# Optimization experiments

Measured on AMD Instinct MI355X. Metric: run time of the kernel, lower is better.

## Reference

```python
import jax, jax.numpy as jnp
import numpy as np

B, T, V, D = 16, 200, 25, 128
N_Q, N_E = 4, 1024
BETA, ALPHA, SLOPE, LN_EPS = 0.25, 0.1, 0.2, 1e-5

def _ring_adjacency(v):
    A = np.zeros((v, v), dtype=np.float32)
    for i in range(v):
        A[i, (i + 1) % v] = 1.0
        A[i, (i - 1) % v] = 1.0
    A = A + np.eye(v, dtype=np.float32)  # A + I, as in module
    d_inv_sqrt = 1.0 / np.sqrt(A.sum(1))
    return (d_inv_sqrt[:, None] * A) * d_inv_sqrt[None, :]

def setup_inputs() -> dict:
    key = jax.random.key(0)
    k_z, k_e, k_w = jax.random.split(key, 3)
    z = jax.random.normal(k_z, (B, T, V, D), dtype=jnp.float32)
    # xavier_uniform for each [n_e, e_dim] codebook
    lim = float(np.sqrt(6.0 / (N_E + D)))
    emb = jax.random.uniform(k_e, (N_Q, N_E, D), dtype=jnp.float32, minval=-lim, maxval=lim)
    wlim = float(np.sqrt(1.0 / D))
    gcn_w = jax.random.uniform(k_w, (D, D), dtype=jnp.float32, minval=-wlim, maxval=wlim)
    return {
        "z": z,
        "emb": emb,
        "A_norm": jnp.asarray(_ring_adjacency(V)),
        "gcn_w": gcn_w,
        "gcn_b": jnp.zeros((D,), jnp.float32),
        "ln_scale": jnp.ones((D,), jnp.float32),
        "ln_bias": jnp.zeros((D,), jnp.float32),
    }

def _gcn_refine(residual, A_norm, gcn_w, gcn_b, ln_scale, ln_bias):
    # residual: [N, V, d]
    neigh = jnp.einsum('vw,nwd->nvd', A_norm, residual)
    neigh = neigh @ gcn_w.T + gcn_b                      # nn.Linear
    neigh = jnp.where(neigh >= 0, neigh, SLOPE * neigh)  # LeakyReLU(0.2)
    mu = neigh.mean(-1, keepdims=True)
    var = ((neigh - mu) ** 2).mean(-1, keepdims=True)
    neigh = (neigh - mu) / jnp.sqrt(var + LN_EPS) * ln_scale + ln_bias
    return residual + ALPHA * neigh

def reference(z, emb, A_norm, gcn_w, gcn_b, ln_scale, ln_bias):
    b, t, v, d = z.shape
    n_q = emb.shape[0]
    zf = z.reshape(b * t, v, d)
    residual = zf
    cum = jnp.zeros_like(zf)
    losses, idxs = [], []
    for k in range(n_q):
        refined = _gcn_refine(residual, A_norm, gcn_w, gcn_b, ln_scale, ln_bias)
        W = emb[k]                               # [n_e, d]
        flat = refined.reshape(-1, d)            # [N*V, d]
        dist = ((flat ** 2).sum(1, keepdims=True)
                - 2.0 * flat @ W.T
                + (W ** 2).sum(1)[None, :])
        idx = jnp.argmin(dist, axis=1)           # [N*V]
        q = W[idx].reshape(b * t, v, d)          # == one_hot @ W
        # commit and codebook terms are identical squared errors -> (1+beta)*mse
        diff = q - jax.lax.stop_gradient(residual)
        losses.append((1.0 + BETA) * (diff ** 2).mean(-1))
        cum = cum + q
        residual = residual - q
        idxs.append(idx.reshape(b * t, v))
    zq = zf + jax.lax.stop_gradient(cum - zf)    # straight-through
    total_loss = jnp.stack(losses, 0).mean()
    indices = jnp.stack(idxs, -1).reshape(b, t, v, n_q)
    return zq.reshape(b, t, v, d), total_loss, indices
```

## Files before the change

kernel.cpp:

```cpp
#include <hip/hip_runtime.h>

#define ZQ_N    10240000
#define IDX_OFF 10240001
#define FLT_BIG 3.402823466e38f

typedef _Float16 f16x8 __attribute__((ext_vector_type(8)));
typedef float    f32x4 __attribute__((ext_vector_type(4)));

__global__ __launch_bounds__(256) void k_wsq(const float* __restrict__ emb,
                                             float* __restrict__ wsq,
                                             float* __restrict__ loss_part) {
    int t = threadIdx.x;
    int g = blockIdx.x * 256 + t;
    if (g < 1024) loss_part[g] = 0.f;
    int row = blockIdx.x * 64 + (t >> 2);
    int seg = t & 3;
    const float4* p = (const float4*)(emb + row * 128 + seg * 32);
    float a = 0.f;
#pragma unroll
    for (int i = 0; i < 8; i++) {
        float4 w = p[i];
        a = fmaf(w.x, w.x, a); a = fmaf(w.y, w.y, a);
        a = fmaf(w.z, w.z, a); a = fmaf(w.w, w.w, a);
    }
    a += __shfl_xor(a, 1);
    a += __shfl_xor(a, 2);
    if (seg == 0) wsq[row] = a;
}

__global__ __launch_bounds__(256) void k_wsplit(const float* __restrict__ emb,
        _Float16* __restrict__ wh, _Float16* __restrict__ wl,
        const float* __restrict__ gw,
        _Float16* __restrict__ gh, _Float16* __restrict__ gl) {
    int c = blockIdx.x * 256 + threadIdx.x;
    int q   = c >> 14;
    int col = (c >> 4) & 1023;
    int k8  = (c & 15) * 8;
    const float* srcp = emb + q * 131072 + col * 128 + k8;
    float4 a = *(const float4*)(srcp);
    float4 b = *(const float4*)(srcp + 4);
    float vv[8] = {a.x, a.y, a.z, a.w, b.x, b.y, b.z, b.w};
    union { _Float16 h[8]; uint4 u4; } ph, pl;
#pragma unroll
    for (int j = 0; j < 8; j++) {
        float v = vv[j] * 1024.f;
        _Float16 h = (_Float16)v;
        float r1 = v - (float)h;
        ph.h[j] = h; pl.h[j] = (_Float16)r1;
    }
    int P  = col >> 7, w = (col >> 5) & 3, ct = (col >> 4) & 1, lm = col & 15;
    int ks = k8 >> 5, quad = (k8 >> 3) & 3;
    int off = (((P * 4 + w) * 4 + ks) * 2 + ct) * 512 + (quad * 16 + lm) * 8;
    *(uint4*)(wh + q * 131072 + off) = ph.u4;
    *(uint4*)(wl + q * 131072 + off) = pl.u4;

    if (c < 16384) {
        float v = gw[c] * 1024.f;
        _Float16 h = (_Float16)v;
        float r1 = v - (float)h;
        gh[c] = h; gl[c] = (_Float16)r1;
    }
}

__global__ __launch_bounds__(256) void k_refine(const float* __restrict__ zbase,
        const float* __restrict__ emb, const float* __restrict__ idx_f, int stage,
        float* __restrict__ refined, float* __restrict__ s_out,
        const float* __restrict__ An,
        const _Float16* __restrict__ gh, const _Float16* __restrict__ gl,
        const float* __restrict__ gb, const float* __restrict__ lsc,
        const float* __restrict__ lbi) {
    __shared__ __align__(16) float Rn[25 * 128];
    __shared__ __align__(16) unsigned char nbuf[2 * 32 * 136 * 2];
    __shared__ float Al[625];
    __shared__ int cds[75];
    _Float16* nh = (_Float16*)nbuf;
    _Float16* nl = (_Float16*)(nbuf + 8704);
    float*    nei = (float*)nbuf;
    const int tid = threadIdx.x;
    const int n = blockIdx.x;

    if (tid < 75) {
        int r = tid / 3, j = tid - r * 3;
        if (j < stage) cds[tid] = (int)idx_f[(n * 25 + r) * 4 + j];
    }
    for (int i = tid; i < 625; i += 256) Al[i] = An[i];
    __syncthreads();

    const float4* zp = (const float4*)(zbase + n * 3200);
    float4* Rn4 = (float4*)Rn;
    for (int i = tid; i < 800; i += 256) {
        float4 rv = zp[i];
        int r = i >> 5, c4 = (i & 31) * 4;
#pragma unroll
        for (int j = 0; j < 3; j++) {
            if (j < stage) {
                const float4 q = *(const float4*)(emb + j * 131072 + cds[r * 3 + j] * 128 + c4);
                rv.x -= q.x; rv.y -= q.y; rv.z -= q.z; rv.w -= q.w;
            }
        }
        Rn4[i] = rv;
    }
    __syncthreads();

    for (int i = tid; i < 512; i += 256) {
        int r = i >> 4, k8 = (i & 15) * 8;
        union { _Float16 h[8]; uint4 u4; } ph, pl;
        if (r < 25) {
            int vm = (r == 0) ? 24 : r - 1;
            int vp = (r == 24) ? 0 : r + 1;
            float am = Al[r * 25 + vm], a0 = Al[r * 25 + r], ap = Al[r * 25 + vp];
#pragma unroll
            for (int j = 0; j < 8; j++) {
                int d = k8 + j;
                float val = am * Rn[vm * 128 + d];
                val = fmaf(a0, Rn[r  * 128 + d], val);
                val = fmaf(ap, Rn[vp * 128 + d], val);
                float v1 = val * 1024.f;
                _Float16 h = (_Float16)v1; float fh = (float)h;
                ph.h[j] = h; pl.h[j] = (_Float16)(v1 - fh);
            }
        } else {
            ph.u4 = make_uint4(0u, 0u, 0u, 0u);
            pl.u4 = make_uint4(0u, 0u, 0u, 0u);
        }
        int off = r * 136 + k8;
        *(uint4*)(&nh[off]) = ph.u4;
        *(uint4*)(&nl[off]) = pl.u4;
    }
    __syncthreads();

    {
        const int lane = tid & 63;
        const int wv   = tid >> 6;
        const int quad = lane >> 4;
        const int lm   = lane & 15;
        const int bbase = (wv * 32 + lm) * 128 + quad * 8;
        const int abase = lm * 136 + quad * 8;

        f32x4 racc[2][2];
#pragma unroll
        for (int a = 0; a < 2; a++)
#pragma unroll
            for (int b = 0; b < 2; b++) racc[a][b] = (f32x4){0.f, 0.f, 0.f, 0.f};

#pragma unroll
        for (int k0 = 0; k0 < 4; k0++) {
            const int ko = k0 * 32;
            f16x8 ah[2], al[2];
#pragma unroll
            for (int mt = 0; mt < 2; mt++) {
                ah[mt] = *(const f16x8*)(&nh[abase + mt * (16 * 136) + ko]);
                al[mt] = *(const f16x8*)(&nl[abase + mt * (16 * 136) + ko]);
            }
            f16x8 bh[2], bl[2];
#pragma unroll
            for (int ct = 0; ct < 2; ct++) {
                bh[ct] = *(const f16x8*)(gh + bbase + ct * (16 * 128) + ko);
                bl[ct] = *(const f16x8*)(gl + bbase + ct * (16 * 128) + ko);
            }
#pragma unroll
            for (int ct = 0; ct < 2; ct++)
#pragma unroll
                for (int mt = 0; mt < 2; mt++)
                    racc[ct][mt] = __builtin_amdgcn_mfma_f32_16x16x32_f16(ah[mt], bh[ct], racc[ct][mt], 0, 0, 0);
#pragma unroll
            for (int ct = 0; ct < 2; ct++)
#pragma unroll
                for (int mt = 0; mt < 2; mt++)
                    racc[ct][mt] = __builtin_amdgcn_mfma_f32_16x16x32_f16(ah[mt], bl[ct], racc[ct][mt], 0, 0, 0);
#pragma unroll
            for (int ct = 0; ct < 2; ct++)
#pragma unroll
                for (int mt = 0; mt < 2; mt++)
                    racc[ct][mt] = __builtin_amdgcn_mfma_f32_16x16x32_f16(al[mt], bh[ct], racc[ct][mt], 0, 0, 0);
        }

        __syncthreads();

#pragma unroll
        for (int ct = 0; ct < 2; ct++)
#pragma unroll
            for (int mt = 0; mt < 2; mt++)
#pragma unroll
                for (int rg = 0; rg < 4; rg++) {
                    int row = mt * 16 + quad * 4 + rg;
                    if (row < 25)
                        nei[row * 132 + wv * 32 + ct * 16 + lm] =
                            racc[ct][mt][rg] * 9.5367431640625e-07f;
                }
    }
    __syncthreads();

    const int dpg = tid & 31;
    const int vs  = tid >> 5;
    const int dp0 = dpg * 4;

    float4 b4  = *(const float4*)(gb + dp0);
    float4 sc4 = *(const float4*)(lsc + dp0);
    float4 bi4 = *(const float4*)(lbi + dp0);
    const float bb[4] = {b4.x, b4.y, b4.z, b4.w};
    const float sc[4] = {sc4.x, sc4.y, sc4.z, sc4.w};
    const float bi[4] = {bi4.x, bi4.y, bi4.z, bi4.w};

#pragma unroll
    for (int i = 0; i < 4; i++) {
        int v = vs + 8 * i;
        if (v >= 25) break;
        float4 y4 = *(const float4*)(&nei[v * 132 + dp0]);
        const float yin[4] = {y4.x, y4.y, y4.z, y4.w};
        float y[4];
#pragma unroll
        for (int c = 0; c < 4; c++) {
            float t = yin[c] + bb[c];
            y[c] = (t >= 0.f) ? t : 0.2f * t;
        }
        float s1 = y[0] + y[1] + y[2] + y[3];
#pragma unroll
        for (int m = 1; m <= 16; m <<= 1) s1 += __shfl_xor(s1, m);
        float mu = s1 * (1.f / 128.f);
        float d2 = 0.f;
#pragma unroll
        for (int c = 0; c < 4; c++) { float t = y[c] - mu; d2 = fmaf(t, t, d2); }
#pragma unroll
        for (int m = 1; m <= 16; m <<= 1) d2 += __shfl_xor(d2, m);
        float inv = 1.f / sqrtf(d2 * (1.f / 128.f) + 1e-5f);

        float4 rn4 = *(const float4*)(&Rn[v * 128 + dp0]);
        const float rn[4] = {rn4.x, rn4.y, rn4.z, rn4.w};
        float o[4];
#pragma unroll
        for (int c = 0; c < 4; c++)
            o[c] = rn[c] + 0.1f * ((y[c] - mu) * inv * sc[c] + bi[c]);

        *(float4*)(refined + (n * 25 + v) * 128 + dp0) =
            make_float4(o[0], o[1], o[2], o[3]);

        float ss = 0.f;
#pragma unroll
        for (int c = 0; c < 4; c++) ss = fmaf(o[c], o[c], ss);
#pragma unroll
        for (int m = 1; m <= 16; m <<= 1) ss += __shfl_xor(ss, m);
        if (dpg == 0) s_out[n * 25 + v] = ss;
    }
}


#define XPAD 140

#define VQ_LOADB(BH, BL, IT) do {                                              \
    const int _o = ((((IT) >> 2) * 4 + w) * 4 + ((IT) & 3)) * 1024 + lane * 8; \
    BH[0] = *(const f16x8*)(wh + _o);        BL[0] = *(const f16x8*)(wl + _o);        \
    BH[1] = *(const f16x8*)(wh + _o + 512);  BL[1] = *(const f16x8*)(wl + _o + 512);  \
} while (0)

#define VQ_STEP(IT, BH, BL) do {                                               \
    const int _ko = abase + ((IT) & 3) * 32;                                   \
    f16x8 _ah[4], _al[4];                                                      \
    _Pragma("unroll")                                                          \
    for (int _rt = 0; _rt < 4; _rt++) {                                        \
        const int _off = _ko + _rt * (16 * XPAD);                              \
        _ah[_rt] = *(const f16x8*)(&xh_s[_off]);                               \
        _al[_rt] = *(const f16x8*)(&xl_s[_off]);                               \
    }                                                                          \
    _Pragma("unroll")                                                          \
    for (int _ct = 0; _ct < 2; _ct++)                                          \
        _Pragma("unroll")                                                      \
        for (int _rt = 0; _rt < 4; _rt++)                                      \
            acc[_ct][_rt] = __builtin_amdgcn_mfma_f32_16x16x32_f16(_ah[_rt], BH[_ct], acc[_ct][_rt], 0, 0, 0); \
    _Pragma("unroll")                                                          \
    for (int _ct = 0; _ct < 2; _ct++)                                          \
        _Pragma("unroll")                                                      \
        for (int _rt = 0; _rt < 4; _rt++)                                      \
            acc[_ct][_rt] = __builtin_amdgcn_mfma_f32_16x16x32_f16(_ah[_rt], BL[_ct], acc[_ct][_rt], 0, 0, 0); \
    _Pragma("unroll")                                                          \
    for (int _ct = 0; _ct < 2; _ct++)                                          \
        _Pragma("unroll")                                                      \
        for (int _rt = 0; _rt < 4; _rt++)                                      \
            acc[_ct][_rt] = __builtin_amdgcn_mfma_f32_16x16x32_f16(_al[_rt], BH[_ct], acc[_ct][_rt], 0, 0, 0); \
} while (0)

#define VQ_EPI(P) do {                                                         \
    float _sr[16];                                                             \
    _Pragma("unroll")                                                          \
    for (int _rt = 0; _rt < 4; _rt++) {                                        \
        float4 _t = *(const float4*)(s_g + row0 + _rt * 16 + quad * 4);        \
        _sr[_rt * 4 + 0] = _t.x; _sr[_rt * 4 + 1] = _t.y;                      \
        _sr[_rt * 4 + 2] = _t.z; _sr[_rt * 4 + 3] = _t.w;                      \
    }                                                                          \
    _Pragma("unroll")                                                          \
    for (int _ct = 0; _ct < 2; _ct++) {                                        \
        const int _col = (P) * 128 + w * 32 + _ct * 16 + lm;                   \
        const float _wq = wsq_k[_col];                                         \
        _Pragma("unroll")                                                      \
        for (int _rt = 0; _rt < 4; _rt++) {                                    \
            _Pragma("unroll")                                                  \
            for (int _rg = 0; _rg < 4; _rg++) {                                \
                float _d = (_sr[_rt * 4 + _rg]                                 \
                            - 1.9073486328125e-06f * acc[_ct][_rt][_rg]) + _wq;\
                int _s = _rt * 4 + _rg;                                        \
                if (_d < bestv[_s]) { bestv[_s] = _d; besti[_s] = _col; }      \
            }                                                                  \
        }                                                                      \
    }                                                                          \
} while (0)

#define FIN_STAGE(K, ACC) do {                                                 \
    const float4 q = *(const float4*)(emb + (K) * 131072 + cds4[r * 4 + (K)] * 128 + c4); \
    float dx = q.x - rv.x, dy = q.y - rv.y, dz = q.z - rv.z, dw = q.w - rv.w;  \
    ACC = fmaf(dx, dx, ACC); ACC = fmaf(dy, dy, ACC);                          \
    ACC = fmaf(dz, dz, ACC); ACC = fmaf(dw, dw, ACC);                          \
    s4.x += q.x; s4.y += q.y; s4.z += q.z; s4.w += q.w;                        \
    rv.x -= q.x; rv.y -= q.y; rv.z -= q.z; rv.w -= q.w;                        \
} while (0)

__global__ __launch_bounds__(256) void k_vq(const float* __restrict__ refined,
        const _Float16* __restrict__ wh,
        const _Float16* __restrict__ wl,
        const float* __restrict__ wsq_k,
        const float* __restrict__ s_g,
        float* __restrict__ idx_out, int stage,
        const float* __restrict__ z, const float* __restrict__ emb,
        float* __restrict__ zq, float* __restrict__ loss_part) {
    __shared__ __align__(16) _Float16 xh_s[64 * XPAD];
    __shared__ __align__(16) _Float16 xl_s[64 * XPAD];
    __shared__ int il[64];
    __shared__ int cds4[256];
    const int tid = threadIdx.x;
    const int row0 = blockIdx.x * 64;

    const int lane = tid & 63;
    const int w    = tid >> 6;
    const int quad = lane >> 4;
    const int lm   = lane & 15;

    const int abase = lm * XPAD + quad * 8;

    f16x8 bha[2], bla[2], bhb[2], blb[2];
    VQ_LOADB(bha, bla, 0);

    for (int i = tid; i < 1024; i += 256) {
        int r = i >> 4, k8 = (i & 15) * 8;
        const float* srcp = refined + (row0 + r) * 128 + k8;
        float4 a = *(const float4*)(srcp);
        float4 b = *(const float4*)(srcp + 4);
        float vv[8] = {a.x, a.y, a.z, a.w, b.x, b.y, b.z, b.w};
        union { _Float16 h[8]; uint4 u4; } ph, pl;
#pragma unroll
        for (int j = 0; j < 8; j++) {
            float v = vv[j] * 1024.f;
            _Float16 h = (_Float16)v; float fh = (float)h;
            float r1 = v - fh;
            ph.h[j] = h; pl.h[j] = (_Float16)r1;
        }
        int off = r * XPAD + k8;
        *(uint4*)(&xh_s[off]) = ph.u4;
        *(uint4*)(&xl_s[off]) = pl.u4;
    }
    __syncthreads();

    float bestv[16];
    int   besti[16];
#pragma unroll
    for (int s = 0; s < 16; s++) { bestv[s] = FLT_BIG; besti[s] = 0; }

    f32x4 acc[2][4];

#pragma unroll
    for (int ith = 0; ith < 16; ith++) {
        const int it0 = ith * 2, it1 = it0 + 1;
        VQ_LOADB(bhb, blb, it1);
        if ((it0 & 3) == 0) {
#pragma unroll
            for (int a = 0; a < 2; a++)
#pragma unroll
                for (int b = 0; b < 4; b++) acc[a][b] = (f32x4){0.f, 0.f, 0.f, 0.f};
        }
        VQ_STEP(it0, bha, bla);
        if (it1 < 31) VQ_LOADB(bha, bla, it1 + 1);
        VQ_STEP(it1, bhb, blb);
        if ((it1 & 3) == 3) VQ_EPI(it1 >> 2);
    }

#pragma unroll
    for (int s = 0; s < 16; s++) {
#pragma unroll
        for (int m = 1; m <= 8; m <<= 1) {
            float ov = __shfl_xor(bestv[s], m);
            int   oi = __shfl_xor(besti[s], m);
            if (ov < bestv[s] || (ov == bestv[s] && oi < besti[s])) {
                bestv[s] = ov; besti[s] = oi;
            }
        }
    }

    __syncthreads();
    float* redv = (float*)xh_s;
    int*   redi = (int*)xl_s;
    if (lm == 0) {
#pragma unroll
        for (int s = 0; s < 16; s++) {
            int row = (s >> 2) * 16 + quad * 4 + (s & 3);
            redv[w * 64 + row] = bestv[s];
            redi[w * 64 + row] = besti[s];
        }
    }
    __syncthreads();
    if (tid < 64) {
        float bv = redv[tid]; int bi = redi[tid];
#pragma unroll
        for (int ww = 1; ww < 4; ww++) {
            float v2 = redv[ww * 64 + tid]; int i2 = redi[ww * 64 + tid];
            if (v2 < bv || (v2 == bv && i2 < bi)) { bv = v2; bi = i2; }
        }
        il[tid] = bi;
        idx_out[(row0 + tid) * 4 + stage] = (float)bi;
    }

    if (stage < 3) return;

    __syncthreads();
    {
        int r = tid >> 2, j = tid & 3;
        cds4[tid] = (j == 3) ? il[r] : (int)idx_out[(row0 + r) * 4 + j];
    }
    __syncthreads();

    const float4* zp = (const float4*)(z + row0 * 128);
    float4* zqp = (float4*)(zq + row0 * 128);
    float a0 = 0.f, a1 = 0.f, a2 = 0.f, a3 = 0.f;
#pragma unroll
    for (int j = 0; j < 8; j++) {
        int idx4 = tid + j * 256;
        int r = idx4 >> 5;
        int c4 = (idx4 & 31) * 4;
        float4 rv = zp[idx4];
        float4 s4 = make_float4(0.f, 0.f, 0.f, 0.f);
        FIN_STAGE(0, a0);
        FIN_STAGE(1, a1);
        FIN_STAGE(2, a2);
        FIN_STAGE(3, a3);
        zqp[idx4] = s4;
    }
#pragma unroll
    for (int m = 1; m <= 32; m <<= 1) {
        a0 += __shfl_xor(a0, m); a1 += __shfl_xor(a1, m);
        a2 += __shfl_xor(a2, m); a3 += __shfl_xor(a3, m);
    }
    if ((tid & 63) == 0) {
        float* slot = &loss_part[blockIdx.x & 1023];
        atomicAdd(slot, a0); atomicAdd(slot, a1);
        atomicAdd(slot, a2); atomicAdd(slot, a3);
    }
}

__global__ __launch_bounds__(256) void k_loss(const float* __restrict__ loss_part,
                                              float* __restrict__ out) {
    int t = threadIdx.x;
    float a = loss_part[t] + loss_part[t + 256] + loss_part[t + 512] + loss_part[t + 768];
#pragma unroll
    for (int m = 1; m <= 32; m <<= 1) a += __shfl_xor(a, m);
    __shared__ float w[4];
    if ((t & 63) == 0) w[t >> 6] = a;
    __syncthreads();
    if (t == 0) {
        float s = w[0] + w[1] + w[2] + w[3];
        out[ZQ_N] = s * (1.25f / (128.f * 320000.f));
    }
}

extern "C" void kernel_launch(void* const* d_in, const int* in_sizes, int n_in,
                              void* d_out, int out_size, void* d_ws, size_t ws_size,
                              hipStream_t stream) {
    (void)in_sizes; (void)n_in; (void)out_size; (void)ws_size;
    const float* z   = (const float*)d_in[0];
    const float* emb = (const float*)d_in[1];
    const float* An  = (const float*)d_in[2];
    const float* gw  = (const float*)d_in[3];
    const float* gb  = (const float*)d_in[4];
    const float* lsc = (const float*)d_in[5];
    const float* lbi = (const float*)d_in[6];

    float* out     = (float*)d_out;
    float* zq      = out;
    float* idx_out = out + IDX_OFF;

    float* ws        = (float*)d_ws;
    float* refined   = ws + 10240000;
    _Float16* gh_f16 = (_Float16*)(ws + 20480000);
    _Float16* gl_f16 = (_Float16*)(ws + 20488192);
    _Float16* wh_f16 = (_Float16*)(ws + 20496384);
    _Float16* wl_f16 = (_Float16*)(ws + 20758528);
    float* s_g       = ws + 21020672;
    float* wsq       = ws + 21100672;
    float* loss_part = ws + 21104768;

    k_wsq<<<64, 256, 0, stream>>>(emb, wsq, loss_part);
    k_wsplit<<<256, 256, 0, stream>>>(emb, wh_f16, wl_f16, gw, gh_f16, gl_f16);
    for (int k = 0; k < 4; k++) {
        k_refine<<<3200, 256, 0, stream>>>(z, emb, idx_out, k,
                                           refined, s_g, An,
                                           gh_f16, gl_f16, gb, lsc, lbi);
        k_vq<<<1250, 256, 0, stream>>>(refined,
                                       wh_f16 + k * 131072, wl_f16 + k * 131072,
                                       wsq + k * 1024,
                                       s_g, idx_out, k,
                                       z, emb, zq, loss_part);
    }
    k_loss<<<1, 256, 0, stream>>>(loss_part, out);
}
```

Measured before the change: 716.9 us.

## Split VQ codebook search across two blocks with 64-bit atomicMin merge

Each VQ block now scans half the 1024-entry codebook, which doubles the grid to 2500 blocks, and the two partial argmins are merged with a 64-bit atomicMin on an order-preserving (distance, index) key. k_refine resets the keys for its stage and reads earlier codes from the key buffer. The final zq, loss and index pass moves out of the last VQ launch into a separate k_final kernel. The intent is more parallelism and occupancy on the GEMM-argmin kernel, at the cost of atomics, one extra launch and reloading X tiles twice.

```diff
diff --git a/kernel.cpp b/kernel.cpp
--- a/kernel.cpp
+++ b/kernel.cpp
@@ -63,7 +63,8 @@
 }
 
 __global__ __launch_bounds__(256) void k_refine(const float* __restrict__ zbase,
-        const float* __restrict__ emb, const float* __restrict__ idx_f, int stage,
+        const float* __restrict__ emb, unsigned long long* __restrict__ keys,
+        int stage,
         float* __restrict__ refined, float* __restrict__ s_out,
         const float* __restrict__ An,
         const _Float16* __restrict__ gh, const _Float16* __restrict__ gl,
@@ -79,9 +80,12 @@
     const int tid = threadIdx.x;
     const int n = blockIdx.x;
 
+    if (tid < 25)
+        keys[(size_t)stage * 80000 + n * 25 + tid] = ~0ull;
     if (tid < 75) {
         int r = tid / 3, j = tid - r * 3;
-        if (j < stage) cds[tid] = (int)idx_f[(n * 25 + r) * 4 + j];
+        if (j < stage)
+            cds[tid] = (int)(keys[(size_t)j * 80000 + n * 25 + r] & 0xFFFFFFFFull);
     }
     for (int i = tid; i < 625; i += 256) Al[i] = An[i];
     __syncthreads();
@@ -248,7 +252,7 @@
 #define XPAD 140
 
 #define VQ_LOADB(BH, BL, IT) do {                                              \
-    const int _o = ((((IT) >> 2) * 4 + w) * 4 + ((IT) & 3)) * 1024 + lane * 8; \
+    const int _o = (((cb4 + ((IT) >> 2)) * 4 + w) * 4 + ((IT) & 3)) * 1024 + lane * 8; \
     BH[0] = *(const f16x8*)(wh + _o);        BL[0] = *(const f16x8*)(wl + _o);        \
     BH[1] = *(const f16x8*)(wh + _o + 512);  BL[1] = *(const f16x8*)(wl + _o + 512);  \
 } while (0)
@@ -289,7 +293,7 @@
     }                                                                          \
     _Pragma("unroll")                                                          \
     for (int _ct = 0; _ct < 2; _ct++) {                                        \
-        const int _col = (P) * 128 + w * 32 + _ct * 16 + lm;                   \
+        const int _col = (cb4 + (P)) * 128 + w * 32 + _ct * 16 + lm;           \
         const float _wq = wsq_k[_col];                                         \
         _Pragma("unroll")                                                      \
         for (int _rt = 0; _rt < 4; _rt++) {                                    \
@@ -304,29 +308,17 @@
     }                                                                          \
 } while (0)
 
-#define FIN_STAGE(K, ACC) do {                                                 \
-    const float4 q = *(const float4*)(emb + (K) * 131072 + cds4[r * 4 + (K)] * 128 + c4); \
-    float dx = q.x - rv.x, dy = q.y - rv.y, dz = q.z - rv.z, dw = q.w - rv.w;  \
-    ACC = fmaf(dx, dx, ACC); ACC = fmaf(dy, dy, ACC);                          \
-    ACC = fmaf(dz, dz, ACC); ACC = fmaf(dw, dw, ACC);                          \
-    s4.x += q.x; s4.y += q.y; s4.z += q.z; s4.w += q.w;                        \
-    rv.x -= q.x; rv.y -= q.y; rv.z -= q.z; rv.w -= q.w;                        \
-} while (0)
-
 __global__ __launch_bounds__(256) void k_vq(const float* __restrict__ refined,
         const _Float16* __restrict__ wh,
         const _Float16* __restrict__ wl,
         const float* __restrict__ wsq_k,
         const float* __restrict__ s_g,
-        float* __restrict__ idx_out, int stage,
-        const float* __restrict__ z, const float* __restrict__ emb,
-        float* __restrict__ zq, float* __restrict__ loss_part) {
+        unsigned long long* __restrict__ keys_k) {
     __shared__ __align__(16) _Float16 xh_s[64 * XPAD];
     __shared__ __align__(16) _Float16 xl_s[64 * XPAD];
-    __shared__ int il[64];
-    __shared__ int cds4[256];
     const int tid = threadIdx.x;
-    const int row0 = blockIdx.x * 64;
+    const int row0 = (blockIdx.x >> 1) * 64;
+    const int cb4  = (blockIdx.x & 1) * 4;
 
     const int lane = tid & 63;
     const int w    = tid >> 6;
@@ -366,7 +358,7 @@
     f32x4 acc[2][4];
 
 #pragma unroll
-    for (int ith = 0; ith < 16; ith++) {
+    for (int ith = 0; ith < 8; ith++) {
         const int it0 = ith * 2, it1 = it0 + 1;
         VQ_LOADB(bhb, blb, it1);
         if ((it0 & 3) == 0) {
@@ -376,7 +368,7 @@
                 for (int b = 0; b < 4; b++) acc[a][b] = (f32x4){0.f, 0.f, 0.f, 0.f};
         }
         VQ_STEP(it0, bha, bla);
-        if (it1 < 31) VQ_LOADB(bha, bla, it1 + 1);
+        if (it1 < 15) VQ_LOADB(bha, bla, it1 + 1);
         VQ_STEP(it1, bhb, blb);
         if ((it1 & 3) == 3) VQ_EPI(it1 >> 2);
     }
@@ -412,16 +404,35 @@
             float v2 = redv[ww * 64 + tid]; int i2 = redi[ww * 64 + tid];
             if (v2 < bv || (v2 == bv && i2 < bi)) { bv = v2; bi = i2; }
         }
-        il[tid] = bi;
-        idx_out[(row0 + tid) * 4 + stage] = (float)bi;
-    }
-
-    if (stage < 3) return;
-
-    __syncthreads();
+        unsigned int u = __float_as_uint(bv);
+        u = (u & 0x80000000u) ? ~u : (u | 0x80000000u);
+        unsigned long long key = ((unsigned long long)u << 32)
+                               | (unsigned long long)(unsigned int)bi;
+        atomicMin(&keys_k[row0 + tid], key);
+    }
+}
+
+#define FIN_STAGE(K, ACC) do {                                                 \
+    const float4 q = *(const float4*)(emb + (K) * 131072 + codes[r * 4 + (K)] * 128 + c4); \
+    float dx = q.x - rv.x, dy = q.y - rv.y, dz = q.z - rv.z, dw = q.w - rv.w;  \
+    ACC = fmaf(dx, dx, ACC); ACC = fmaf(dy, dy, ACC);                          \
+    ACC = fmaf(dz, dz, ACC); ACC = fmaf(dw, dw, ACC);                          \
+    s4.x += q.x; s4.y += q.y; s4.z += q.z; s4.w += q.w;                        \
+    rv.x -= q.x; rv.y -= q.y; rv.z -= q.z; rv.w -= q.w;                        \
+} while (0)
+
+__global__ __launch_bounds__(256) void k_final(const float* __restrict__ z,
+        const float* __restrict__ emb, const unsigned long long* __restrict__ keys,
+        float* __restrict__ idx_out,
+        float* __restrict__ zq, float* __restrict__ loss_part) {
+    __shared__ int codes[256];
+    const int tid = threadIdx.x;
+    const int row0 = blockIdx.x * 64;
     {
         int r = tid >> 2, j = tid & 3;
-        cds4[tid] = (j == 3) ? il[r] : (int)idx_out[(row0 + r) * 4 + j];
+        int c = (int)(keys[(size_t)j * 80000 + row0 + r] & 0xFFFFFFFFull);
+        codes[tid] = c;
+        idx_out[(row0 + r) * 4 + j] = (float)c;
     }
     __syncthreads();
 
@@ -485,6 +496,7 @@
     float* idx_out = out + IDX_OFF;
 
     float* ws        = (float*)d_ws;
+    unsigned long long* keys = (unsigned long long*)ws;
     float* refined   = ws + 10240000;
     _Float16* gh_f16 = (_Float16*)(ws + 20480000);
     _Float16* gl_f16 = (_Float16*)(ws + 20488192);
@@ -497,14 +509,14 @@
     k_wsq<<<64, 256, 0, stream>>>(emb, wsq, loss_part);
     k_wsplit<<<256, 256, 0, stream>>>(emb, wh_f16, wl_f16, gw, gh_f16, gl_f16);
     for (int k = 0; k < 4; k++) {
-        k_refine<<<3200, 256, 0, stream>>>(z, emb, idx_out, k,
+        k_refine<<<3200, 256, 0, stream>>>(z, emb, keys, k,
                                            refined, s_g, An,
                                            gh_f16, gl_f16, gb, lsc, lbi);
-        k_vq<<<1250, 256, 0, stream>>>(refined,
+        k_vq<<<2500, 256, 0, stream>>>(refined,
                                        wh_f16 + k * 131072, wl_f16 + k * 131072,
                                        wsq + k * 1024,
-                                       s_g, idx_out, k,
-                                       z, emb, zq, loss_part);
-    }
+                                       s_g, keys + (size_t)k * 80000);
+    }
+    k_final<<<1250, 256, 0, stream>>>(z, emb, keys, idx_out, zq, loss_part);
     k_loss<<<1, 256, 0, stream>>>(loss_part, out);
 }
```

Result: slower. 906.4 us (+26.4%).
